# Kernel tuning notes

Measured on AMD Instinct MI355X. Metric: run time of the kernel, lower is better.

Reference implementation:

```python
import jax, jax.numpy as jnp
import numpy as np

N = 50000      # nodes
E = 640000     # edges
DIN = 256      # in_channels
DE = 64        # edge_dim
H1 = 128       # hidden_channels (conv1 out)
H2 = 64        # hidden_channels//2 (conv2 out)
OUT = 1


def tconv(x, src, dst, edge_attr, Wq, bq, Wk, bk, Wv, bv, We, Ws, bs):
    """PyG TransformerConv, heads=1, concat=True, root_weight=True."""
    n = x.shape[0]
    C = Wq.shape[1]
    q = x @ Wq + bq                      # [N, C]
    k = x @ Wk + bk                      # [N, C]
    v = x @ Wv + bv                      # [N, C]
    e = edge_attr @ We                   # [E, C] (lin_edge has no bias)
    k_e = k[src] + e                     # key_j + edge_emb per edge
    alpha = jnp.sum(q[dst] * k_e, axis=-1) / jnp.sqrt(jnp.float32(C))  # [E]
    # neighborhood softmax over incoming edges of each dst node
    m = jax.ops.segment_max(alpha, dst, num_segments=n)
    ex = jnp.exp(alpha - m[dst])
    denom = jax.ops.segment_sum(ex, dst, num_segments=n)
    a = ex / (denom[dst] + 1e-16)
    msg = a[:, None] * (v[src] + e)      # [E, C]
    out = jax.ops.segment_sum(msg, dst, num_segments=n)  # [N, C]
    return out + x @ Ws + bs             # root/skip connection


def setup_inputs() -> dict:
    key = jax.random.key(0)
    ks = jax.random.split(key, 24)
    p = lambda k, shape: jax.random.normal(k, shape, jnp.float32) * 0.02
    inp = {
        "x": jax.random.normal(ks[0], (N, DIN), jnp.float32),
        "edge_index": jax.random.randint(ks[1], (2, E), 0, N),
        "edge_attr": jax.random.normal(ks[2], (E, DE), jnp.float32),
        # conv1 params (in=DIN -> out=H1)
        "Wq1": p(ks[3], (DIN, H1)), "bq1": jnp.zeros((H1,), jnp.float32),
        "Wk1": p(ks[4], (DIN, H1)), "bk1": jnp.zeros((H1,), jnp.float32),
        "Wv1": p(ks[5], (DIN, H1)), "bv1": jnp.zeros((H1,), jnp.float32),
        "We1": p(ks[6], (DE, H1)),
        "Ws1": p(ks[7], (DIN, H1)), "bs1": jnp.zeros((H1,), jnp.float32),
        # conv2 params (in=H1 -> out=H2)
        "Wq2": p(ks[8], (H1, H2)), "bq2": jnp.zeros((H2,), jnp.float32),
        "Wk2": p(ks[9], (H1, H2)), "bk2": jnp.zeros((H2,), jnp.float32),
        "Wv2": p(ks[10], (H1, H2)), "bv2": jnp.zeros((H2,), jnp.float32),
        "We2": p(ks[11], (DE, H2)),
        "Ws2": p(ks[12], (H1, H2)), "bs2": jnp.zeros((H2,), jnp.float32),
        # classifier
        "Wc": p(ks[13], (H2, OUT)), "bc": jnp.zeros((OUT,), jnp.float32),
    }
    return inp


def reference(x, edge_index, edge_attr,
              Wq1, bq1, Wk1, bk1, Wv1, bv1, We1, Ws1, bs1,
              Wq2, bq2, Wk2, bk2, Wv2, bv2, We2, Ws2, bs2,
              Wc, bc):
    src, dst = edge_index[0], edge_index[1]
    h = tconv(x, src, dst, edge_attr, Wq1, bq1, Wk1, bk1, Wv1, bv1, We1, Ws1, bs1)
    h = jax.nn.relu(h)  # dropout is identity in eval mode
    h = tconv(h, src, dst, edge_attr, Wq2, bq2, Wk2, bk2, Wv2, bv2, We2, Ws2, bs2)
    h = jax.nn.relu(h)
    return h @ Wc + bc  # [N, 1] logits
```

## Files before the change

kernel.cpp:

```cpp
#include <hip/hip_runtime.h>
#include <math.h>

constexpr int NN  = 50000;
constexpr int NE  = 640000;
constexpr int DIN = 256;
constexpr int DE  = 64;
constexpr int H1  = 128;
constexpr int H2  = 64;
constexpr int EWS = H1 + H2;

using u16 = unsigned short;
typedef __attribute__((ext_vector_type(8))) short bf16x8;
typedef __attribute__((ext_vector_type(4))) float f32x4;

__device__ inline u16 f2bf(float f) {
  unsigned u = __float_as_uint(f);
  unsigned r = (u + 0x7FFFu + ((u >> 16) & 1u)) >> 16;
  return (u16)r;
}
__device__ inline float bf2f(u16 h) { return __uint_as_float(((unsigned)h) << 16); }
__device__ inline unsigned pack2(u16 a, u16 b) {
  return (unsigned)a | ((unsigned)b << 16);
}
__device__ inline f32x4 mfma16(bf16x8 a, bf16x8 b, f32x4 c) {
  return __builtin_amdgcn_mfma_f32_16x16x32_bf16(a, b, c, 0, 0, 0);
}

__global__ __launch_bounds__(256) void packwt_kernel(
    const float* __restrict__ W0, const float* __restrict__ W1,
    const float* __restrict__ W2, const float* __restrict__ W3,
    const float* __restrict__ b0, const float* __restrict__ b1,
    const float* __restrict__ b2, const float* __restrict__ b3,
    u16* __restrict__ Bth, u16* __restrict__ Btl, float* __restrict__ bcat,
    int K, int C, int nmats) {
  int total = nmats * C * K;
  for (int idx = blockIdx.x * blockDim.x + threadIdx.x; idx < total;
       idx += gridDim.x * blockDim.x) {
    int k = idx % K;
    int n = idx / K;
    int which = n / C, cc = n % C;
    const float* W = which == 0 ? W0 : which == 1 ? W1 : which == 2 ? W2 : W3;
    float v = W[k * C + cc];
    u16 h = f2bf(v);
    Bth[(size_t)n * K + k] = h;
    Btl[(size_t)n * K + k] = f2bf(v - bf2f(h));
    if (k == 0 && bcat) {
      const float* b = which == 0 ? b0 : which == 1 ? b1 : which == 2 ? b2 : b3;
      bcat[n] = b ? b[cc] : 0.f;
    }
  }
}

__global__ __launch_bounds__(256) void hist_kernel(const int* __restrict__ dst,
                                                   int* __restrict__ deg, int nE) {
  int e = blockIdx.x * blockDim.x + threadIdx.x;
  if (e < nE) atomicAdd(&deg[dst[e]], 1);
}

__global__ __launch_bounds__(256) void scan1_kernel(const int* __restrict__ deg,
                                                    int* __restrict__ part,
                                                    int* __restrict__ chunkSums,
                                                    int n) {
  __shared__ int s[256];
  int tid = threadIdx.x;
  int i = blockIdx.x * 256 + tid;
  int v0 = (i < n) ? deg[i] : 0;
  s[tid] = v0;
  __syncthreads();
  for (int off = 1; off < 256; off <<= 1) {
    int v = (tid >= off) ? s[tid - off] : 0;
    __syncthreads();
    s[tid] += v;
    __syncthreads();
  }
  if (i < n) part[i] = s[tid];
  if (tid == 255) chunkSums[blockIdx.x] = s[255];
}

__global__ __launch_bounds__(256) void scan2_kernel(int* __restrict__ chunkSums,
                                                    int nchunks) {
  __shared__ int s[256];
  int tid = threadIdx.x;
  s[tid] = (tid < nchunks) ? chunkSums[tid] : 0;
  __syncthreads();
  for (int off = 1; off < 256; off <<= 1) {
    int v = (tid >= off) ? s[tid - off] : 0;
    __syncthreads();
    s[tid] += v;
    __syncthreads();
  }
  if (tid < nchunks) chunkSums[tid] = s[tid];
}

__global__ __launch_bounds__(256) void scan3_kernel(const int* __restrict__ deg,
                                                    const int* __restrict__ part,
                                                    const int* __restrict__ chunkSums,
                                                    int* __restrict__ row_start,
                                                    int n, int nE) {
  int i = blockIdx.x * 256 + threadIdx.x;
  if (i < n)
    row_start[i] = part[i] - deg[i] + (blockIdx.x ? chunkSums[blockIdx.x - 1] : 0);
  if (i == 0) row_start[n] = nE;
}

__global__ __launch_bounds__(256) void scatter_kernel(const int* __restrict__ dst,
                                                      const int* __restrict__ row_start,
                                                      int* __restrict__ cursor,
                                                      int* __restrict__ eid, int nE) {
  int e = blockIdx.x * blockDim.x + threadIdx.x;
  if (e >= nE) return;
  int d = dst[e];
  int pos = row_start[d] + atomicAdd(&cursor[d], 1);
  eid[pos] = e;
}

__global__ __launch_bounds__(256) void sort_extract_kernel(
    int* __restrict__ eid, const int* __restrict__ row_start,
    const int* __restrict__ srcI, int* __restrict__ src_csr, int n) {
  int v = blockIdx.x * blockDim.x + threadIdx.x;
  if (v >= n) return;
  int b = row_start[v], e = row_start[v + 1];
  for (int i = b + 1; i < e; i++) {
    int key = eid[i];
    int j = i - 1;
    while (j >= b && eid[j] > key) { eid[j + 1] = eid[j]; j--; }
    eid[j + 1] = key;
  }
  for (int i = b; i < e; i++) src_csr[i] = srcI[eid[i]];
}

template <int BN, int EPI>
__global__ __launch_bounds__(256) void mfma_gemm_kernel(
    const float* __restrict__ A, const int* __restrict__ ridx,
    const u16* __restrict__ Bth, const u16* __restrict__ Btl,
    const float* __restrict__ bias, float* __restrict__ Cout,
    float* __restrict__ Qp, u16* __restrict__ KVp, float* __restrict__ Sp,
    int M, int Nn, int K, int Cl) {
  constexpr int BM = 128, BK = 32;
  constexpr int NI = BN / 32;
  constexpr int SM_STAGE = (BM + BN) * BK * 2;
  constexpr int SM_EPI = (EPI >= 1) ? BM * BN : 0;
  constexpr int SM = SM_STAGE > SM_EPI ? SM_STAGE : SM_EPI;
  __shared__ __align__(16) u16 smem[SM];
  u16* Ah = smem;
  u16* Al = smem + BM * BK;
  u16* Bh = smem + 2 * BM * BK;
  u16* Bl = smem + 2 * BM * BK + BN * BK;
  int tid = threadIdx.x;
  int lane = tid & 63, wid = tid >> 6;
  int wm = wid >> 1, wn = wid & 1;
  int row0 = blockIdx.y * BM, col0 = blockIdx.x * BN;
  int k8 = lane >> 4, rb = lane & 15;

  f32x4 acc[4][NI];
#pragma unroll
  for (int mi = 0; mi < 4; mi++)
#pragma unroll
    for (int ni = 0; ni < NI; ni++) acc[mi][ni] = (f32x4){0.f, 0.f, 0.f, 0.f};

  size_t aoff[2];
  int sdst[2];
  for (int p = 0; p < 2; p++) {
    int idx = p * 256 + tid;
    int r = idx >> 2, c = idx & 3;
    int ar = row0 + r;
    if (ar >= M) ar = M - 1;
    if (ridx) ar = ridx[ar];
    aoff[p] = (size_t)ar * K + c * 8;
    sdst[p] = r * BK + ((c ^ ((r >> 1) & 3)) << 3);
  }

  for (int k0 = 0; k0 < K; k0 += BK) {
    __syncthreads();
#pragma unroll
    for (int p = 0; p < 2; p++) {
      const float* s = A + aoff[p] + k0;
      float4 u = *(const float4*)s, v = *(const float4*)(s + 4);
      float f[8] = {u.x, u.y, u.z, u.w, v.x, v.y, v.z, v.w};
      u16 h[8], l[8];
#pragma unroll
      for (int j = 0; j < 8; j++) {
        h[j] = f2bf(f[j]);
        l[j] = f2bf(f[j] - bf2f(h[j]));
      }
      *(uint4*)&Ah[sdst[p]] = make_uint4(pack2(h[0], h[1]), pack2(h[2], h[3]),
                                         pack2(h[4], h[5]), pack2(h[6], h[7]));
      *(uint4*)&Al[sdst[p]] = make_uint4(pack2(l[0], l[1]), pack2(l[2], l[3]),
                                         pack2(l[4], l[5]), pack2(l[6], l[7]));
    }
#pragma unroll
    for (int p = 0; p < (BN * 4) / 256; p++) {
      int idx = p * 256 + tid;
      int n = idx >> 2, c = idx & 3;
      size_t goff = (size_t)(col0 + n) * K + k0 + c * 8;
      int doff = n * BK + ((c ^ ((n >> 1) & 3)) << 3);
      *(uint4*)&Bh[doff] = *(const uint4*)&Bth[goff];
      *(uint4*)&Bl[doff] = *(const uint4*)&Btl[goff];
    }
    __syncthreads();
    bf16x8 ah[4], al[4], bh[NI], bl[NI];
#pragma unroll
    for (int mi = 0; mi < 4; mi++) {
      int row = wm * 64 + mi * 16 + rb;
      int off = row * BK + ((k8 ^ ((row >> 1) & 3)) << 3);
      ah[mi] = *(const bf16x8*)&Ah[off];
      al[mi] = *(const bf16x8*)&Al[off];
    }
#pragma unroll
    for (int ni = 0; ni < NI; ni++) {
      int cn = wn * (BN / 2) + ni * 16 + rb;
      int off = cn * BK + ((k8 ^ ((cn >> 1) & 3)) << 3);
      bh[ni] = *(const bf16x8*)&Bh[off];
      bl[ni] = *(const bf16x8*)&Bl[off];
    }
#pragma unroll
    for (int mi = 0; mi < 4; mi++)
#pragma unroll
      for (int ni = 0; ni < NI; ni++) {
        f32x4 c = acc[mi][ni];
        c = mfma16(ah[mi], bh[ni], c);
        c = mfma16(al[mi], bh[ni], c);
        c = mfma16(ah[mi], bl[ni], c);
        acc[mi][ni] = c;
      }
  }

  bool kvseg = false;
  if constexpr (EPI == 2) {
    int seg = col0 / Cl;
    kvseg = (seg == 1 || seg == 2);
    if (!kvseg) {
      float* dst = (seg == 0) ? Qp : Sp;
      int cbase = (seg == 0) ? col0 : col0 - 3 * Cl;
#pragma unroll
      for (int ni = 0; ni < NI; ni++) {
        int cfrag = wn * (BN / 2) + ni * 16 + rb;
        float bv = bias ? bias[col0 + cfrag] : 0.f;
#pragma unroll
        for (int mi = 0; mi < 4; mi++) {
#pragma unroll
          for (int q = 0; q < 4; q++) {
            int row = row0 + wm * 64 + mi * 16 + k8 * 4 + q;
            if (row < M)
              dst[(size_t)row * Cl + cbase + cfrag] = acc[mi][ni][q] + bv;
          }
        }
      }
      return;
    }
  }
  if (EPI == 1 || kvseg) {
    __syncthreads();
    u16* S = smem;
#pragma unroll
    for (int ni = 0; ni < NI; ni++) {
      int coll = wn * (BN / 2) + ni * 16 + rb;
      float bv = bias ? bias[col0 + coll] : 0.f;
#pragma unroll
      for (int mi = 0; mi < 4; mi++) {
#pragma unroll
        for (int q = 0; q < 4; q++) {
          int rowl = wm * 64 + mi * 16 + k8 * 4 + q;
          S[rowl * BN + (coll ^ (((rowl >> 2) & 3) << 4))] =
              f2bf(acc[mi][ni][q] + bv);
        }
      }
    }
    __syncthreads();
    u16* dbase;
    size_t dstride;
    int dcol0;
    if constexpr (EPI == 2) {
      dbase = KVp; dstride = 2 * Cl; dcol0 = col0 - Cl;
    } else {
      dbase = (u16*)Cout; dstride = Nn; dcol0 = col0;
    }
    constexpr int PASSES = (BM * BN * 2) / (256 * 16);
#pragma unroll
    for (int p = 0; p < PASSES; p++) {
      int idx = p * 256 + tid;
      int r = idx / (BN / 8);
      int cp = idx % (BN / 8);
      int row = row0 + r;
      int cps = cp ^ (((r >> 2) & 3) << 1);
      if (row < M)
        *(uint4*)&dbase[(size_t)row * dstride + dcol0 + cp * 8] =
            *(const uint4*)&S[r * BN + cps * 8];
    }
    return;
  }
  if constexpr (EPI == 0) {
#pragma unroll
    for (int ni = 0; ni < NI; ni++) {
      int col = col0 + wn * (BN / 2) + ni * 16 + rb;
      float bv = bias ? bias[col] : 0.f;
#pragma unroll
      for (int mi = 0; mi < 4; mi++) {
#pragma unroll
        for (int q = 0; q < 4; q++) {
          int row = row0 + wm * 64 + mi * 16 + k8 * 4 + q;
          if (row < M) Cout[(size_t)row * Nn + col] = acc[mi][ni][q] + bv;
        }
      }
    }
  }
}

template <int C, int EOFF>
__global__ __launch_bounds__(256) void fused_edge_kernel(
    const float* __restrict__ Q, const float* __restrict__ SKIP,
    const u16* __restrict__ KV, const u16* __restrict__ Ew,
    const int* __restrict__ row_start, const int* __restrict__ src_csr,
    float* __restrict__ h, float scale, int n) {
  constexpr int CPL = C / 64;
  int node = blockIdx.x * 4 + (threadIdx.x >> 6);
  int lane = threadIdx.x & 63;
  if (node >= n) return;
  int ch = lane * CPL;
  float q[CPL], acc[CPL], skip[CPL];
#pragma unroll
  for (int j = 0; j < CPL; j++) {
    q[j] = Q[(size_t)node * C + ch + j];
    skip[j] = SKIP[(size_t)node * C + ch + j];
    acc[j] = 0.f;
  }
  float m = -INFINITY, denom = 0.f;
  int b = row_start[node], e = row_start[node + 1];
  for (int i = b; i < e; i += 4) {
    float part[4], vv[4][CPL];
#pragma unroll
    for (int u = 0; u < 4; u++) {
      int idx = (i + u < e) ? i + u : e - 1;
      int s = src_csr[idx];
      const u16* kvp = KV + (size_t)s * (2 * C);
      const u16* Ee = Ew + (size_t)idx * EWS + EOFF;
      float kk[CPL], ev[CPL];
      if constexpr (CPL == 2) {
        unsigned uk = *(const unsigned*)(kvp + ch);
        unsigned uv = *(const unsigned*)(kvp + C + ch);
        unsigned ue = *(const unsigned*)(Ee + ch);
        kk[0] = bf2f((u16)uk); kk[1] = bf2f((u16)(uk >> 16));
        vv[u][0] = bf2f((u16)uv); vv[u][1] = bf2f((u16)(uv >> 16));
        ev[0] = bf2f((u16)ue); ev[1] = bf2f((u16)(ue >> 16));
      } else {
        kk[0] = bf2f(kvp[ch]);
        vv[u][0] = bf2f(kvp[C + ch]);
        ev[0] = bf2f(Ee[ch]);
      }
      float p = 0.f;
#pragma unroll
      for (int j = 0; j < CPL; j++) {
        p = fmaf(q[j], kk[j] + ev[j], p);
        vv[u][j] += ev[j];
      }
      part[u] = p;
    }
#pragma unroll
    for (int off = 32; off > 0; off >>= 1) {
      part[0] += __shfl_xor(part[0], off);
      part[1] += __shfl_xor(part[1], off);
      part[2] += __shfl_xor(part[2], off);
      part[3] += __shfl_xor(part[3], off);
    }
    float l[4];
#pragma unroll
    for (int u = 0; u < 4; u++)
      l[u] = (i + u < e) ? part[u] * scale : -INFINITY;
    float nm = fmaxf(fmaxf(fmaxf(l[0], l[1]), fmaxf(l[2], l[3])), m);
    float f = expf(m - nm);
    float w[4];
#pragma unroll
    for (int u = 0; u < 4; u++) w[u] = expf(l[u] - nm);
    denom = denom * f + (w[0] + w[1]) + (w[2] + w[3]);
#pragma unroll
    for (int j = 0; j < CPL; j++) {
      float a = acc[j] * f;
      a = fmaf(w[0], vv[0][j], a);
      a = fmaf(w[1], vv[1][j], a);
      a = fmaf(w[2], vv[2][j], a);
      a = fmaf(w[3], vv[3][j], a);
      acc[j] = a;
    }
    m = nm;
  }
  float inv = 1.f / (denom + 1e-16f);
#pragma unroll
  for (int j = 0; j < CPL; j++)
    h[(size_t)node * C + ch + j] = fmaxf(acc[j] * inv + skip[j], 0.f);
}

__global__ __launch_bounds__(256) void classifier_kernel(
    const float* __restrict__ h2, const float* __restrict__ Wc,
    const float* __restrict__ bc, float* __restrict__ out, int n) {
  int w = blockIdx.x * 4 + (threadIdx.x >> 6);
  int lane = threadIdx.x & 63;
  if (w >= n) return;
  float v = h2[(size_t)w * 64 + lane] * Wc[lane];
#pragma unroll
  for (int off = 32; off > 0; off >>= 1) v += __shfl_xor(v, off);
  if (lane == 0) out[w] = v + bc[0];
}

extern "C" void kernel_launch(void* const* d_in, const int* in_sizes, int n_in,
                              void* d_out, int out_size, void* d_ws,
                              size_t ws_size, hipStream_t stream) {
  const float* x         = (const float*)d_in[0];
  const int*   ei        = (const int*)d_in[1];
  const float* edge_attr = (const float*)d_in[2];
  const float* Wq1 = (const float*)d_in[3];  const float* bq1 = (const float*)d_in[4];
  const float* Wk1 = (const float*)d_in[5];  const float* bk1 = (const float*)d_in[6];
  const float* Wv1 = (const float*)d_in[7];  const float* bv1 = (const float*)d_in[8];
  const float* We1 = (const float*)d_in[9];
  const float* Ws1 = (const float*)d_in[10]; const float* bs1 = (const float*)d_in[11];
  const float* Wq2 = (const float*)d_in[12]; const float* bq2 = (const float*)d_in[13];
  const float* Wk2 = (const float*)d_in[14]; const float* bk2 = (const float*)d_in[15];
  const float* Wv2 = (const float*)d_in[16]; const float* bv2 = (const float*)d_in[17];
  const float* We2 = (const float*)d_in[18];
  const float* Ws2 = (const float*)d_in[19]; const float* bs2 = (const float*)d_in[20];
  const float* Wc  = (const float*)d_in[21]; const float* bc  = (const float*)d_in[22];
  float* out = (float*)d_out;

  const int* srcI = ei;
  const int* dstI = ei + NE;

  char* ws = (char*)d_ws;
  size_t off = 0;
  auto alloc = [&](size_t bytes) {
    void* p = ws + off;
    off += (bytes + 255) & ~(size_t)255;
    return p;
  };
  u16*   EwB  = (u16*)alloc((size_t)NE * EWS * 2);
  float* Q1   = (float*)alloc((size_t)NN * H1 * 4);
  float* S1   = (float*)alloc((size_t)NN * H1 * 4);
  u16*   KV1  = (u16*)alloc((size_t)NN * 2 * H1 * 2);
  float* Q2   = (float*)alloc((size_t)NN * H2 * 4);
  float* S2   = (float*)alloc((size_t)NN * H2 * 4);
  u16*   KV2  = (u16*)alloc((size_t)NN * 2 * H2 * 2);
  float* h1   = (float*)alloc((size_t)NN * H1 * 4);
  float* h2   = (float*)alloc((size_t)NN * H2 * 4);
  u16* B1h = (u16*)alloc((size_t)4 * H1 * DIN * 2);
  u16* B1l = (u16*)alloc((size_t)4 * H1 * DIN * 2);
  u16* B2h = (u16*)alloc((size_t)4 * H2 * H1 * 2);
  u16* B2l = (u16*)alloc((size_t)4 * H2 * H1 * 2);
  u16* Ech = (u16*)alloc((size_t)EWS * DE * 2);
  u16* Ecl = (u16*)alloc((size_t)EWS * DE * 2);
  float* b1cat = (float*)alloc(4 * H1 * 4);
  float* b2cat = (float*)alloc(4 * H2 * 4);
  int* deg       = (int*)alloc(NN * 4);
  int* cursor    = (int*)alloc(NN * 4);
  int* row_start = (int*)alloc((NN + 1) * 4);
  int* part      = (int*)alloc(((NN + 255) / 256) * 256 * 4);
  int* chunkSums = (int*)alloc(256 * 4);
  int* eid       = (int*)alloc(NE * 4);
  int* src_csr   = (int*)alloc(NE * 4);
  (void)ws_size; (void)in_sizes; (void)n_in; (void)out_size;

  const int nchunks = (NN + 255) / 256;

  packwt_kernel<<<256, 256, 0, stream>>>(Wq1, Wk1, Wv1, Ws1, bq1, bk1, bv1, bs1,
                                         B1h, B1l, b1cat, DIN, H1, 4);
  packwt_kernel<<<128, 256, 0, stream>>>(Wq2, Wk2, Wv2, Ws2, bq2, bk2, bv2, bs2,
                                         B2h, B2l, b2cat, H1, H2, 4);
  packwt_kernel<<<64, 256, 0, stream>>>(We1, nullptr, nullptr, nullptr, nullptr,
                                        nullptr, nullptr, nullptr, Ech, Ecl,
                                        nullptr, DE, H1, 1);
  packwt_kernel<<<32, 256, 0, stream>>>(We2, nullptr, nullptr, nullptr, nullptr,
                                        nullptr, nullptr, nullptr,
                                        Ech + (size_t)H1 * DE, Ecl + (size_t)H1 * DE,
                                        nullptr, DE, H2, 1);

  hipMemsetAsync(deg, 0, NN * sizeof(int), stream);
  hipMemsetAsync(cursor, 0, NN * sizeof(int), stream);
  hist_kernel<<<(NE + 255) / 256, 256, 0, stream>>>(dstI, deg, NE);
  scan1_kernel<<<nchunks, 256, 0, stream>>>(deg, part, chunkSums, NN);
  scan2_kernel<<<1, 256, 0, stream>>>(chunkSums, nchunks);
  scan3_kernel<<<nchunks, 256, 0, stream>>>(deg, part, chunkSums, row_start, NN, NE);
  scatter_kernel<<<(NE + 255) / 256, 256, 0, stream>>>(dstI, row_start, cursor,
                                                       eid, NE);
  sort_extract_kernel<<<(NN + 255) / 256, 256, 0, stream>>>(eid, row_start, srcI,
                                                            src_csr, NN);

  mfma_gemm_kernel<192, 1><<<dim3(1, NE / 128), 256, 0, stream>>>(
      edge_attr, eid, Ech, Ecl, nullptr, (float*)EwB,
      nullptr, nullptr, nullptr, NE, EWS, DE, 0);

  mfma_gemm_kernel<64, 2><<<dim3(4 * H1 / 64, (NN + 127) / 128), 256, 0, stream>>>(
      x, nullptr, B1h, B1l, b1cat, nullptr, Q1, KV1, S1, NN, 4 * H1, DIN, H1);
  fused_edge_kernel<H1, 0><<<(NN + 3) / 4, 256, 0, stream>>>(
      Q1, S1, KV1, EwB, row_start, src_csr, h1, 0.08838834764831845f, NN);

  mfma_gemm_kernel<64, 2><<<dim3(4 * H2 / 64, (NN + 127) / 128), 256, 0, stream>>>(
      h1, nullptr, B2h, B2l, b2cat, nullptr, Q2, KV2, S2, NN, 4 * H2, H1, H2);
  fused_edge_kernel<H2, H1><<<(NN + 3) / 4, 256, 0, stream>>>(
      Q2, S2, KV2, EwB, row_start, src_csr, h2, 0.125f, NN);

  classifier_kernel<<<(NN + 3) / 4, 256, 0, stream>>>(h2, Wc, bc, out, NN);
}
```

Baseline: 548.4 us.

## Add dedicated 256-row edge-embedding GEMM kernel and widen node GEMM tile

Replaces the generic MFMA GEMM used for the edge-attribute projection with a specialised kernel: 512 threads, 256-row tiles, the full 192-column output per block, and a two-half shared-memory epilogue that writes bf16 rows with no bounds checks. It also raises the column tile of the conv1 node projection GEMM from 64 to 128. The aim is to reuse the gathered A rows and B tiles across more outputs and to cut block count and launch overhead. The cost is more registers and shared memory per block, which may lower occupancy. The generic kernel loses its EPI==1 path.

```diff
diff --git a/kernel.cpp b/kernel.cpp
--- a/kernel.cpp
+++ b/kernel.cpp
@@ -249,7 +249,7 @@
       return;
     }
   }
-  if (EPI == 1 || kvseg) {
+  if (kvseg) {
     __syncthreads();
     u16* S = smem;
 #pragma unroll
@@ -267,14 +267,9 @@
       }
     }
     __syncthreads();
-    u16* dbase;
-    size_t dstride;
-    int dcol0;
-    if constexpr (EPI == 2) {
-      dbase = KVp; dstride = 2 * Cl; dcol0 = col0 - Cl;
-    } else {
-      dbase = (u16*)Cout; dstride = Nn; dcol0 = col0;
-    }
+    u16* dbase = KVp;
+    size_t dstride = 2 * Cl;
+    int dcol0 = col0 - Cl;
     constexpr int PASSES = (BM * BN * 2) / (256 * 16);
 #pragma unroll
     for (int p = 0; p < PASSES; p++) {
@@ -302,6 +297,129 @@
           if (row < M) Cout[(size_t)row * Nn + col] = acc[mi][ni][q] + bv;
         }
       }
+    }
+  }
+}
+
+__global__ __launch_bounds__(512) void edge_gemm_kernel(
+    const float* __restrict__ A, const int* __restrict__ ridx,
+    const u16* __restrict__ Bth, const u16* __restrict__ Btl,
+    u16* __restrict__ Cbf) {
+  constexpr int BM = 256, BN = 192, BK = 32, K = DE;
+  constexpr int NI = 6;
+  __shared__ __align__(16) u16 smem[(BM + BN) * BK * 2];
+  u16* Ah = smem;
+  u16* Al = smem + BM * BK;
+  u16* Bh = smem + 2 * BM * BK;
+  u16* Bl = smem + 2 * BM * BK + BN * BK;
+  int tid = threadIdx.x;
+  int lane = tid & 63, wid = tid >> 6;
+  int wm = wid >> 1, wn = wid & 1;
+  int row0 = blockIdx.x * BM;
+  int k8 = lane >> 4, rb = lane & 15;
+
+  f32x4 acc[4][NI];
+#pragma unroll
+  for (int mi = 0; mi < 4; mi++)
+#pragma unroll
+    for (int ni = 0; ni < NI; ni++) acc[mi][ni] = (f32x4){0.f, 0.f, 0.f, 0.f};
+
+  size_t aoff[2];
+  int sdst[2];
+#pragma unroll
+  for (int p = 0; p < 2; p++) {
+    int idx = p * 512 + tid;
+    int r = idx >> 2, c = idx & 3;
+    int ar = ridx[row0 + r];
+    aoff[p] = (size_t)ar * K + c * 8;
+    sdst[p] = r * BK + ((c ^ ((r >> 1) & 3)) << 3);
+  }
+
+  for (int k0 = 0; k0 < K; k0 += BK) {
+    __syncthreads();
+#pragma unroll
+    for (int p = 0; p < 2; p++) {
+      const float* s = A + aoff[p] + k0;
+      float4 u = *(const float4*)s, v = *(const float4*)(s + 4);
+      float f[8] = {u.x, u.y, u.z, u.w, v.x, v.y, v.z, v.w};
+      u16 h[8], l[8];
+#pragma unroll
+      for (int j = 0; j < 8; j++) {
+        h[j] = f2bf(f[j]);
+        l[j] = f2bf(f[j] - bf2f(h[j]));
+      }
+      *(uint4*)&Ah[sdst[p]] = make_uint4(pack2(h[0], h[1]), pack2(h[2], h[3]),
+                                         pack2(h[4], h[5]), pack2(h[6], h[7]));
+      *(uint4*)&Al[sdst[p]] = make_uint4(pack2(l[0], l[1]), pack2(l[2], l[3]),
+                                         pack2(l[4], l[5]), pack2(l[6], l[7]));
+    }
+#pragma unroll
+    for (int p = 0; p < 2; p++) {
+      int idx = p * 512 + tid;
+      if (idx < BN * 4) {
+        int n = idx >> 2, c = idx & 3;
+        size_t goff = (size_t)n * K + k0 + c * 8;
+        int doff = n * BK + ((c ^ ((n >> 1) & 3)) << 3);
+        *(uint4*)&Bh[doff] = *(const uint4*)&Bth[goff];
+        *(uint4*)&Bl[doff] = *(const uint4*)&Btl[goff];
+      }
+    }
+    __syncthreads();
+    bf16x8 ah[4], al[4], bh[NI], bl[NI];
+#pragma unroll
+    for (int mi = 0; mi < 4; mi++) {
+      int row = wm * 64 + mi * 16 + rb;
+      int off = row * BK + ((k8 ^ ((row >> 1) & 3)) << 3);
+      ah[mi] = *(const bf16x8*)&Ah[off];
+      al[mi] = *(const bf16x8*)&Al[off];
+    }
+#pragma unroll
+    for (int ni = 0; ni < NI; ni++) {
+      int cn = wn * 96 + ni * 16 + rb;
+      int off = cn * BK + ((k8 ^ ((cn >> 1) & 3)) << 3);
+      bh[ni] = *(const bf16x8*)&Bh[off];
+      bl[ni] = *(const bf16x8*)&Bl[off];
+    }
+#pragma unroll
+    for (int mi = 0; mi < 4; mi++)
+#pragma unroll
+      for (int ni = 0; ni < NI; ni++) {
+        f32x4 c = acc[mi][ni];
+        c = mfma16(ah[mi], bh[ni], c);
+        c = mfma16(al[mi], bh[ni], c);
+        c = mfma16(ah[mi], bl[ni], c);
+        acc[mi][ni] = c;
+      }
+  }
+
+  u16* S = smem;
+#pragma unroll
+  for (int half = 0; half < 2; half++) {
+    __syncthreads();
+    if ((wm >> 1) == half) {
+#pragma unroll
+      for (int ni = 0; ni < NI; ni++) {
+        int coll = wn * 96 + ni * 16 + rb;
+#pragma unroll
+        for (int mi = 0; mi < 4; mi++) {
+#pragma unroll
+          for (int q = 0; q < 4; q++) {
+            int rowl = (wm & 1) * 64 + mi * 16 + k8 * 4 + q;
+            S[rowl * BN + (coll ^ (((rowl >> 2) & 3) << 4))] =
+                f2bf(acc[mi][ni][q]);
+          }
+        }
+      }
+    }
+    __syncthreads();
+#pragma unroll
+    for (int p = 0; p < 6; p++) {
+      int idx = p * 512 + tid;
+      int r = idx / (BN / 8);
+      int cp = idx % (BN / 8);
+      int row = row0 + half * 128 + r;
+      int cps = cp ^ (((r >> 2) & 3) << 1);
+      *(uint4*)&Cbf[(size_t)row * BN + cp * 8] = *(const uint4*)&S[r * BN + cps * 8];
     }
   }
 }
@@ -481,11 +599,9 @@
   sort_extract_kernel<<<(NN + 255) / 256, 256, 0, stream>>>(eid, row_start, srcI,
                                                             src_csr, NN);
 
-  mfma_gemm_kernel<192, 1><<<dim3(1, NE / 128), 256, 0, stream>>>(
-      edge_attr, eid, Ech, Ecl, nullptr, (float*)EwB,
-      nullptr, nullptr, nullptr, NE, EWS, DE, 0);
-
-  mfma_gemm_kernel<64, 2><<<dim3(4 * H1 / 64, (NN + 127) / 128), 256, 0, stream>>>(
+  edge_gemm_kernel<<<NE / 256, 512, 0, stream>>>(edge_attr, eid, Ech, Ecl, EwB);
+
+  mfma_gemm_kernel<128, 2><<<dim3(4 * H1 / 128, (NN + 127) / 128), 256, 0, stream>>>(
       x, nullptr, B1h, B1l, b1cat, nullptr, Q1, KV1, S1, NN, 4 * H1, DIN, H1);
   fused_edge_kernel<H1, 0><<<(NN + 3) / 4, 256, 0, stream>>>(
       Q1, S1, KV1, EwB, row_start, src_csr, h1, 0.08838834764831845f, NN);
```

Result: faster. 505.7 us (-7.8%).

## Fold edge projection algebraically into per-node queries and aggregated edge attributes

Applied to the files above, without the earlier changes.

Stops materializing the per-edge projected edge features (E x 192 bf16). The score term q·(e W_e) is rewritten as (q W_e^T)·e, and the message term sum a·(e W_e) as (sum a·e) W_e. The fused edge kernel now gathers raw 64-wide edge_attr rows through eid and accumulates a weighted edge-attr sum per node. Small per-node GEMMs compute QE before the edge kernel and apply W_e after it, with the skip add and ReLU fused into that second GEMM's epilogue. This removes the large edge GEMM and its write/read traffic, at the cost of extra node-level GEMMs and an indirect fp32 gather of edge attributes in each layer. The edge unroll factor also grows from 4 to 8.

```diff
diff --git a/kernel.cpp b/kernel.cpp
--- a/kernel.cpp
+++ b/kernel.cpp
@@ -7,7 +7,6 @@
 constexpr int DE  = 64;
 constexpr int H1  = 128;
 constexpr int H2  = 64;
-constexpr int EWS = H1 + H2;
 
 using u16 = unsigned short;
 typedef __attribute__((ext_vector_type(8))) short bf16x8;
@@ -43,11 +42,23 @@
     float v = W[k * C + cc];
     u16 h = f2bf(v);
     Bth[(size_t)n * K + k] = h;
-    Btl[(size_t)n * K + k] = f2bf(v - bf2f(h));
+    if (Btl) Btl[(size_t)n * K + k] = f2bf(v - bf2f(h));
     if (k == 0 && bcat) {
       const float* b = which == 0 ? b0 : which == 1 ? b1 : which == 2 ? b2 : b3;
       bcat[n] = b ? b[cc] : 0.f;
     }
+  }
+}
+
+__global__ __launch_bounds__(256) void splitcopy_kernel(
+    const float* __restrict__ W, u16* __restrict__ Bh, u16* __restrict__ Bl,
+    int count) {
+  int i = blockIdx.x * blockDim.x + threadIdx.x;
+  if (i < count) {
+    float v = W[i];
+    u16 h = f2bf(v);
+    Bh[i] = h;
+    Bl[i] = f2bf(v - bf2f(h));
   }
 }
 
@@ -135,11 +146,11 @@
     const u16* __restrict__ Bth, const u16* __restrict__ Btl,
     const float* __restrict__ bias, float* __restrict__ Cout,
     float* __restrict__ Qp, u16* __restrict__ KVp, float* __restrict__ Sp,
-    int M, int Nn, int K, int Cl) {
+    const float* __restrict__ Cin, int M, int Nn, int K, int Cl) {
   constexpr int BM = 128, BK = 32;
   constexpr int NI = BN / 32;
   constexpr int SM_STAGE = (BM + BN) * BK * 2;
-  constexpr int SM_EPI = (EPI >= 1) ? BM * BN : 0;
+  constexpr int SM_EPI = (EPI == 2) ? BM * BN : 0;
   constexpr int SM = SM_STAGE > SM_EPI ? SM_STAGE : SM_EPI;
   __shared__ __align__(16) u16 smem[SM];
   u16* Ah = smem;
@@ -189,13 +200,15 @@
                                          pack2(l[4], l[5]), pack2(l[6], l[7]));
     }
 #pragma unroll
-    for (int p = 0; p < (BN * 4) / 256; p++) {
+    for (int p = 0; p < (BN * 4 + 255) / 256; p++) {
       int idx = p * 256 + tid;
-      int n = idx >> 2, c = idx & 3;
-      size_t goff = (size_t)(col0 + n) * K + k0 + c * 8;
-      int doff = n * BK + ((c ^ ((n >> 1) & 3)) << 3);
-      *(uint4*)&Bh[doff] = *(const uint4*)&Bth[goff];
-      *(uint4*)&Bl[doff] = *(const uint4*)&Btl[goff];
+      if (idx < BN * 4) {
+        int n = idx >> 2, c = idx & 3;
+        size_t goff = (size_t)(col0 + n) * K + k0 + c * 8;
+        int doff = n * BK + ((c ^ ((n >> 1) & 3)) << 3);
+        *(uint4*)&Bh[doff] = *(const uint4*)&Bth[goff];
+        *(uint4*)&Bl[doff] = *(const uint4*)&Btl[goff];
+      }
     }
     __syncthreads();
     bf16x8 ah[4], al[4], bh[NI], bl[NI];
@@ -249,7 +262,7 @@
       return;
     }
   }
-  if (EPI == 1 || kvseg) {
+  if (kvseg) {
     __syncthreads();
     u16* S = smem;
 #pragma unroll
@@ -267,14 +280,9 @@
       }
     }
     __syncthreads();
-    u16* dbase;
-    size_t dstride;
-    int dcol0;
-    if constexpr (EPI == 2) {
-      dbase = KVp; dstride = 2 * Cl; dcol0 = col0 - Cl;
-    } else {
-      dbase = (u16*)Cout; dstride = Nn; dcol0 = col0;
-    }
+    u16* dbase = KVp;
+    size_t dstride = 2 * Cl;
+    int dcol0 = col0 - Cl;
     constexpr int PASSES = (BM * BN * 2) / (256 * 16);
 #pragma unroll
     for (int p = 0; p < PASSES; p++) {
@@ -289,104 +297,117 @@
     }
     return;
   }
-  if constexpr (EPI == 0) {
+  if constexpr (EPI == 0 || EPI == 3) {
 #pragma unroll
     for (int ni = 0; ni < NI; ni++) {
       int col = col0 + wn * (BN / 2) + ni * 16 + rb;
-      float bv = bias ? bias[col] : 0.f;
+      float bv = (EPI == 0 && bias) ? bias[col] : 0.f;
 #pragma unroll
       for (int mi = 0; mi < 4; mi++) {
 #pragma unroll
         for (int q = 0; q < 4; q++) {
           int row = row0 + wm * 64 + mi * 16 + k8 * 4 + q;
-          if (row < M) Cout[(size_t)row * Nn + col] = acc[mi][ni][q] + bv;
+          if (row < M) {
+            if constexpr (EPI == 3) {
+              float hv = acc[mi][ni][q] + Cin[(size_t)row * Nn + col];
+              Cout[(size_t)row * Nn + col] = fmaxf(hv, 0.f);
+            } else {
+              Cout[(size_t)row * Nn + col] = acc[mi][ni][q] + bv;
+            }
+          }
         }
       }
     }
   }
 }
 
-template <int C, int EOFF>
+template <int C>
 __global__ __launch_bounds__(256) void fused_edge_kernel(
-    const float* __restrict__ Q, const float* __restrict__ SKIP,
-    const u16* __restrict__ KV, const u16* __restrict__ Ew,
-    const int* __restrict__ row_start, const int* __restrict__ src_csr,
-    float* __restrict__ h, float scale, int n) {
+    const float* __restrict__ Q, const float* __restrict__ QE,
+    const float* __restrict__ SKIP, const u16* __restrict__ KV,
+    const float* __restrict__ EAttr, const int* __restrict__ row_start,
+    const int* __restrict__ src_csr, const int* __restrict__ eid,
+    float* __restrict__ Hp, float* __restrict__ EA, float scale, int n) {
   constexpr int CPL = C / 64;
+  constexpr int EB = 8;
   int node = blockIdx.x * 4 + (threadIdx.x >> 6);
   int lane = threadIdx.x & 63;
   if (node >= n) return;
   int ch = lane * CPL;
-  float q[CPL], acc[CPL], skip[CPL];
+  float q[CPL], accv[CPL], skip[CPL];
 #pragma unroll
   for (int j = 0; j < CPL; j++) {
     q[j] = Q[(size_t)node * C + ch + j];
     skip[j] = SKIP[(size_t)node * C + ch + j];
-    acc[j] = 0.f;
-  }
+    accv[j] = 0.f;
+  }
+  float qe = QE[(size_t)node * DE + lane];
+  float acc_ea = 0.f;
   float m = -INFINITY, denom = 0.f;
   int b = row_start[node], e = row_start[node + 1];
-  for (int i = b; i < e; i += 4) {
-    float part[4], vv[4][CPL];
-#pragma unroll
-    for (int u = 0; u < 4; u++) {
+  for (int i = b; i < e; i += EB) {
+    float part[EB], vv[EB][CPL], eaf[EB];
+#pragma unroll
+    for (int u = 0; u < EB; u++) {
       int idx = (i + u < e) ? i + u : e - 1;
       int s = src_csr[idx];
+      int eo = eid[idx];
       const u16* kvp = KV + (size_t)s * (2 * C);
-      const u16* Ee = Ew + (size_t)idx * EWS + EOFF;
-      float kk[CPL], ev[CPL];
+      eaf[u] = EAttr[(size_t)eo * DE + lane];
+      float kk[CPL];
       if constexpr (CPL == 2) {
         unsigned uk = *(const unsigned*)(kvp + ch);
         unsigned uv = *(const unsigned*)(kvp + C + ch);
-        unsigned ue = *(const unsigned*)(Ee + ch);
         kk[0] = bf2f((u16)uk); kk[1] = bf2f((u16)(uk >> 16));
         vv[u][0] = bf2f((u16)uv); vv[u][1] = bf2f((u16)(uv >> 16));
-        ev[0] = bf2f((u16)ue); ev[1] = bf2f((u16)(ue >> 16));
       } else {
         kk[0] = bf2f(kvp[ch]);
         vv[u][0] = bf2f(kvp[C + ch]);
-        ev[0] = bf2f(Ee[ch]);
-      }
-      float p = 0.f;
-#pragma unroll
-      for (int j = 0; j < CPL; j++) {
-        p = fmaf(q[j], kk[j] + ev[j], p);
-        vv[u][j] += ev[j];
-      }
+      }
+      float p = qe * eaf[u];
+#pragma unroll
+      for (int j = 0; j < CPL; j++) p = fmaf(q[j], kk[j], p);
       part[u] = p;
     }
 #pragma unroll
     for (int off = 32; off > 0; off >>= 1) {
-      part[0] += __shfl_xor(part[0], off);
-      part[1] += __shfl_xor(part[1], off);
-      part[2] += __shfl_xor(part[2], off);
-      part[3] += __shfl_xor(part[3], off);
-    }
-    float l[4];
-#pragma unroll
-    for (int u = 0; u < 4; u++)
+#pragma unroll
+      for (int u = 0; u < EB; u++) part[u] += __shfl_xor(part[u], off);
+    }
+    float l[EB];
+#pragma unroll
+    for (int u = 0; u < EB; u++)
       l[u] = (i + u < e) ? part[u] * scale : -INFINITY;
-    float nm = fmaxf(fmaxf(fmaxf(l[0], l[1]), fmaxf(l[2], l[3])), m);
+    float bm = l[0];
+#pragma unroll
+    for (int u = 1; u < EB; u++) bm = fmaxf(bm, l[u]);
+    float nm = fmaxf(bm, m);
     float f = expf(m - nm);
-    float w[4];
-#pragma unroll
-    for (int u = 0; u < 4; u++) w[u] = expf(l[u] - nm);
-    denom = denom * f + (w[0] + w[1]) + (w[2] + w[3]);
+    float w[EB];
+#pragma unroll
+    for (int u = 0; u < EB; u++) w[u] = expf(l[u] - nm);
+    float wsum = 0.f;
+#pragma unroll
+    for (int u = 0; u < EB; u++) wsum += w[u];
+    denom = denom * f + wsum;
 #pragma unroll
     for (int j = 0; j < CPL; j++) {
-      float a = acc[j] * f;
-      a = fmaf(w[0], vv[0][j], a);
-      a = fmaf(w[1], vv[1][j], a);
-      a = fmaf(w[2], vv[2][j], a);
-      a = fmaf(w[3], vv[3][j], a);
-      acc[j] = a;
-    }
+      float a = accv[j] * f;
+#pragma unroll
+      for (int u = 0; u < EB; u++) a = fmaf(w[u], vv[u][j], a);
+      accv[j] = a;
+    }
+    float ae = acc_ea * f;
+#pragma unroll
+    for (int u = 0; u < EB; u++) ae = fmaf(w[u], eaf[u], ae);
+    acc_ea = ae;
     m = nm;
   }
   float inv = 1.f / (denom + 1e-16f);
 #pragma unroll
   for (int j = 0; j < CPL; j++)
-    h[(size_t)node * C + ch + j] = fmaxf(acc[j] * inv + skip[j], 0.f);
+    Hp[(size_t)node * C + ch + j] = accv[j] * inv + skip[j];
+  EA[(size_t)node * DE + lane] = acc_ea * inv;
 }
 
 __global__ __launch_bounds__(256) void classifier_kernel(
@@ -430,21 +451,32 @@
     off += (bytes + 255) & ~(size_t)255;
     return p;
   };
-  u16*   EwB  = (u16*)alloc((size_t)NE * EWS * 2);
   float* Q1   = (float*)alloc((size_t)NN * H1 * 4);
   float* S1   = (float*)alloc((size_t)NN * H1 * 4);
   u16*   KV1  = (u16*)alloc((size_t)NN * 2 * H1 * 2);
   float* Q2   = (float*)alloc((size_t)NN * H2 * 4);
   float* S2   = (float*)alloc((size_t)NN * H2 * 4);
   u16*   KV2  = (u16*)alloc((size_t)NN * 2 * H2 * 2);
+  float* QE1  = (float*)alloc((size_t)NN * DE * 4);
+  float* QE2  = (float*)alloc((size_t)NN * DE * 4);
+  float* EA1  = (float*)alloc((size_t)NN * DE * 4);
+  float* EA2  = (float*)alloc((size_t)NN * DE * 4);
+  float* Hp1  = (float*)alloc((size_t)NN * H1 * 4);
+  float* Hp2  = (float*)alloc((size_t)NN * H2 * 4);
   float* h1   = (float*)alloc((size_t)NN * H1 * 4);
   float* h2   = (float*)alloc((size_t)NN * H2 * 4);
   u16* B1h = (u16*)alloc((size_t)4 * H1 * DIN * 2);
   u16* B1l = (u16*)alloc((size_t)4 * H1 * DIN * 2);
   u16* B2h = (u16*)alloc((size_t)4 * H2 * H1 * 2);
   u16* B2l = (u16*)alloc((size_t)4 * H2 * H1 * 2);
-  u16* Ech = (u16*)alloc((size_t)EWS * DE * 2);
-  u16* Ecl = (u16*)alloc((size_t)EWS * DE * 2);
+  u16* W1eh = (u16*)alloc((size_t)DE * H1 * 2);
+  u16* W1el = (u16*)alloc((size_t)DE * H1 * 2);
+  u16* W2eh = (u16*)alloc((size_t)DE * H2 * 2);
+  u16* W2el = (u16*)alloc((size_t)DE * H2 * 2);
+  u16* T1h = (u16*)alloc((size_t)H1 * DE * 2);
+  u16* T1l = (u16*)alloc((size_t)H1 * DE * 2);
+  u16* T2h = (u16*)alloc((size_t)H2 * DE * 2);
+  u16* T2l = (u16*)alloc((size_t)H2 * DE * 2);
   float* b1cat = (float*)alloc(4 * H1 * 4);
   float* b2cat = (float*)alloc(4 * H2 * 4);
   int* deg       = (int*)alloc(NN * 4);
@@ -462,12 +494,15 @@
                                          B1h, B1l, b1cat, DIN, H1, 4);
   packwt_kernel<<<128, 256, 0, stream>>>(Wq2, Wk2, Wv2, Ws2, bq2, bk2, bv2, bs2,
                                          B2h, B2l, b2cat, H1, H2, 4);
+  splitcopy_kernel<<<(DE * H1 + 255) / 256, 256, 0, stream>>>(We1, W1eh, W1el,
+                                                              DE * H1);
+  splitcopy_kernel<<<(DE * H2 + 255) / 256, 256, 0, stream>>>(We2, W2eh, W2el,
+                                                              DE * H2);
   packwt_kernel<<<64, 256, 0, stream>>>(We1, nullptr, nullptr, nullptr, nullptr,
-                                        nullptr, nullptr, nullptr, Ech, Ecl,
+                                        nullptr, nullptr, nullptr, T1h, T1l,
                                         nullptr, DE, H1, 1);
   packwt_kernel<<<32, 256, 0, stream>>>(We2, nullptr, nullptr, nullptr, nullptr,
-                                        nullptr, nullptr, nullptr,
-                                        Ech + (size_t)H1 * DE, Ecl + (size_t)H1 * DE,
+                                        nullptr, nullptr, nullptr, T2h, T2l,
                                         nullptr, DE, H2, 1);
 
   hipMemsetAsync(deg, 0, NN * sizeof(int), stream);
@@ -481,19 +516,33 @@
   sort_extract_kernel<<<(NN + 255) / 256, 256, 0, stream>>>(eid, row_start, srcI,
                                                             src_csr, NN);
 
-  mfma_gemm_kernel<192, 1><<<dim3(1, NE / 128), 256, 0, stream>>>(
-      edge_attr, eid, Ech, Ecl, nullptr, (float*)EwB,
-      nullptr, nullptr, nullptr, NE, EWS, DE, 0);
-
-  mfma_gemm_kernel<64, 2><<<dim3(4 * H1 / 64, (NN + 127) / 128), 256, 0, stream>>>(
-      x, nullptr, B1h, B1l, b1cat, nullptr, Q1, KV1, S1, NN, 4 * H1, DIN, H1);
-  fused_edge_kernel<H1, 0><<<(NN + 3) / 4, 256, 0, stream>>>(
-      Q1, S1, KV1, EwB, row_start, src_csr, h1, 0.08838834764831845f, NN);
-
-  mfma_gemm_kernel<64, 2><<<dim3(4 * H2 / 64, (NN + 127) / 128), 256, 0, stream>>>(
-      h1, nullptr, B2h, B2l, b2cat, nullptr, Q2, KV2, S2, NN, 4 * H2, H1, H2);
-  fused_edge_kernel<H2, H1><<<(NN + 3) / 4, 256, 0, stream>>>(
-      Q2, S2, KV2, EwB, row_start, src_csr, h2, 0.125f, NN);
+  const int MB = (NN + 127) / 128;
+
+  mfma_gemm_kernel<128, 2><<<dim3(4 * H1 / 128, MB), 256, 0, stream>>>(
+      x, nullptr, B1h, B1l, b1cat, nullptr, Q1, KV1, S1, nullptr, NN, 4 * H1,
+      DIN, H1);
+  mfma_gemm_kernel<64, 0><<<dim3(1, MB), 256, 0, stream>>>(
+      Q1, nullptr, W1eh, W1el, nullptr, QE1, nullptr, nullptr, nullptr, nullptr,
+      NN, DE, H1, 0);
+  fused_edge_kernel<H1><<<(NN + 3) / 4, 256, 0, stream>>>(
+      Q1, QE1, S1, KV1, edge_attr, row_start, src_csr, eid, Hp1, EA1,
+      0.08838834764831845f, NN);
+  mfma_gemm_kernel<128, 3><<<dim3(1, MB), 256, 0, stream>>>(
+      EA1, nullptr, T1h, T1l, nullptr, h1, nullptr, nullptr, nullptr, Hp1, NN,
+      H1, DE, 0);
+
+  mfma_gemm_kernel<64, 2><<<dim3(4 * H2 / 64, MB), 256, 0, stream>>>(
+      h1, nullptr, B2h, B2l, b2cat, nullptr, Q2, KV2, S2, nullptr, NN, 4 * H2,
+      H1, H2);
+  mfma_gemm_kernel<64, 0><<<dim3(1, MB), 256, 0, stream>>>(
+      Q2, nullptr, W2eh, W2el, nullptr, QE2, nullptr, nullptr, nullptr, nullptr,
+      NN, DE, H2, 0);
+  fused_edge_kernel<H2><<<(NN + 3) / 4, 256, 0, stream>>>(
+      Q2, QE2, S2, KV2, edge_attr, row_start, src_csr, eid, Hp2, EA2, 0.125f,
+      NN);
+  mfma_gemm_kernel<64, 3><<<dim3(1, MB), 256, 0, stream>>>(
+      EA2, nullptr, T2h, T2l, nullptr, h2, nullptr, nullptr, nullptr, Hp2, NN,
+      H2, DE, 0);
 
   classifier_kernel<<<(NN + 3) / 4, 256, 0, stream>>>(h2, Wc, bc, out, NN);
 }
```

Result: faster. 500.8 us (-8.7%).
